# Performance work log

Hardware: AMD Instinct MI355X
Metric: run time of the kernel (lower is better)

## Reference

```python
import jax, jax.numpy as jnp
import numpy as np

N_NODES = 512
IN_FEATURES = 512
N_HEADS = 8
N_HIDDEN = 64  # out_features // n_heads
NEG_SLOPE = 0.2


def setup_inputs() -> dict:
    key = jax.random.key(0)
    k_h, k_ws, k_wt, k_a, k_adj = jax.random.split(key, 5)
    lim_w = 1.0 / np.sqrt(IN_FEATURES)
    lim_a = 1.0 / np.sqrt(N_HIDDEN)
    h = jax.random.normal(k_h, (1, N_NODES, IN_FEATURES), dtype=jnp.float32)
    # nn.Linear weights: [out, in]
    W_source = jax.random.uniform(k_ws, (N_HEADS * N_HIDDEN, IN_FEATURES), jnp.float32, -lim_w, lim_w)
    W_target = jax.random.uniform(k_wt, (N_HEADS * N_HIDDEN, IN_FEATURES), jnp.float32, -lim_w, lim_w)
    attn_w = jax.random.uniform(k_a, (N_HIDDEN,), jnp.float32, -lim_a, lim_a)  # Linear(n_hidden, 1)
    adjacency_matrix = jax.random.randint(k_adj, (N_NODES, N_NODES, 1), 0, 2, dtype=jnp.int32)
    return {"h": h, "W_source": W_source, "W_target": W_target,
            "attn_w": attn_w, "adjacency_matrix": adjacency_matrix}


def reference(h, W_source, W_target, attn_w, adjacency_matrix):
    n_nodes = h.shape[1]
    x = h[0]  # [N, D]; module assumes batch == 1
    g_source = (x @ W_source.T).reshape(n_nodes, N_HEADS, N_HIDDEN)  # [N,H,F]
    g_target = (x @ W_target.T).reshape(n_nodes, N_HEADS, N_HIDDEN)  # [N,H,F]
    # g_sum[i, j] = g_source[j] + g_target[i]  (repeat / repeat_interleave semantics)
    g_sum = g_source[None, :, :, :] + g_target[:, None, :, :]  # [N,N,H,F]
    act = jnp.where(g_sum >= 0, g_sum, NEG_SLOPE * g_sum)       # LeakyReLU
    scores = jnp.einsum('ijhf,f->ijh', act, attn_w)              # [N,N,H]
    scores = jnp.where(adjacency_matrix == 0, -jnp.inf, scores)  # adj broadcasts over heads
    attention = jax.nn.softmax(scores, axis=1)                   # softmax over source nodes j
    # dropout p applied at eval -> identity
    head_output = jnp.einsum('ijh,jhf->ihf', attention, g_target)  # [N,H,F]
    out = head_output.reshape(n_nodes, N_HEADS * N_HIDDEN)         # is_concat=True
    return out, attention
```

## Files before the change

### kernel.cpp

```cpp
#include <hip/hip_runtime.h>

#define NN 512
#define IND 512
#define NH 8
#define NF 64

__global__ __launch_bounds__(256) void transpose512(
    const float* __restrict__ X, float* __restrict__ Xt,
    const float* __restrict__ Wtg, float* __restrict__ Wtg_t)
{
    const float* src = blockIdx.z ? Wtg : X;
    float* dst       = blockIdx.z ? Wtg_t : Xt;
    __shared__ float tile[32][33];
    const int tid = threadIdx.x;
    const int tx = tid & 31, ty4 = (tid >> 5) * 4;
    const int x  = blockIdx.x * 32 + tx;
    const int y0 = blockIdx.y * 32 + ty4;
    #pragma unroll
    for (int r = 0; r < 4; ++r)
        tile[ty4 + r][tx] = src[(size_t)(y0 + r) * NN + x];
    __syncthreads();
    const int xo  = blockIdx.y * 32 + tx;
    const int yo0 = blockIdx.x * 32 + ty4;
    #pragma unroll
    for (int r = 0; r < 4; ++r)
        dst[(size_t)(yo0 + r) * NN + xo] = tile[tx][ty4 + r];
}

__global__ __launch_bounds__(256) void gemm_tn(
    const float* __restrict__ Sa, const float* __restrict__ Va, float* __restrict__ Ca,
    const float* __restrict__ Sb, const float* __restrict__ Vb, float* __restrict__ Cb)
{
    const float* S = blockIdx.z ? Sb : Sa;
    const float* V = blockIdx.z ? Vb : Va;
    float*       C = blockIdx.z ? Cb : Ca;

    __shared__ float2 sp[2][4][64];

    const int tid  = threadIdx.x;
    const int wv   = __builtin_amdgcn_readfirstlane(tid >> 6);
    const int lane = tid & 63;
    const int rg = wv & 1, kh = wv >> 1;
    const int r0 = blockIdx.y * 8 + rg * 4;
    const int c0 = blockIdx.x * 128 + lane * 2;

    const float* Sp = S + (size_t)r0 * IND + kh * 256;
    const float* Vp = V + (size_t)kh * 256 * NN + c0;

    float2 a0 = {0.f, 0.f}, a1 = {0.f, 0.f}, a2 = {0.f, 0.f}, a3 = {0.f, 0.f};
    #pragma unroll 8
    for (int k = 0; k < 256; ++k) {
        float2 v = *reinterpret_cast<const float2*>(Vp + (size_t)k * NN);
        float s0 = Sp[k];
        float s1 = Sp[IND + k];
        float s2 = Sp[2 * IND + k];
        float s3 = Sp[3 * IND + k];
        a0.x = fmaf(s0, v.x, a0.x); a0.y = fmaf(s0, v.y, a0.y);
        a1.x = fmaf(s1, v.x, a1.x); a1.y = fmaf(s1, v.y, a1.y);
        a2.x = fmaf(s2, v.x, a2.x); a2.y = fmaf(s2, v.y, a2.y);
        a3.x = fmaf(s3, v.x, a3.x); a3.y = fmaf(s3, v.y, a3.y);
    }
    if (kh) {
        sp[rg][0][lane] = a0; sp[rg][1][lane] = a1;
        sp[rg][2][lane] = a2; sp[rg][3][lane] = a3;
    }
    __syncthreads();
    if (!kh) {
        float2 p;
        p = sp[rg][0][lane]; a0.x += p.x; a0.y += p.y;
        p = sp[rg][1][lane]; a1.x += p.x; a1.y += p.y;
        p = sp[rg][2][lane]; a2.x += p.x; a2.y += p.y;
        p = sp[rg][3][lane]; a3.x += p.x; a3.y += p.y;
        *reinterpret_cast<float2*>(C + (size_t)(r0 + 0) * NN + c0) = a0;
        *reinterpret_cast<float2*>(C + (size_t)(r0 + 1) * NN + c0) = a1;
        *reinterpret_cast<float2*>(C + (size_t)(r0 + 2) * NN + c0) = a2;
        *reinterpret_cast<float2*>(C + (size_t)(r0 + 3) * NN + c0) = a3;
    }
}

__global__ __launch_bounds__(256) void gat_attn(
    const float* __restrict__ Gs_t,
    const float* __restrict__ Gt,
    const float* __restrict__ attn_w,
    const int*   __restrict__ adj,
    float* __restrict__ out_feat,
    float* __restrict__ out_att)
{
    __shared__ float s_sc[4][512];
    __shared__ float s_red[4][4][64];

    const int tid = threadIdx.x;
    const int i0  = blockIdx.x * 4;
    const int h   = blockIdx.y;

    {
        const int jj = tid * 2;
        float2 acc0 = {0.f,0.f}, acc1 = {0.f,0.f}, acc2 = {0.f,0.f}, acc3 = {0.f,0.f};
        const float* gsp = Gs_t + (size_t)h * NF * NN + jj;
        const float* gtp = Gt + (size_t)i0 * IND + h * NF;
        #pragma unroll 4
        for (int f = 0; f < NF; ++f) {
            float w  = attn_w[f];
            float w6 = 0.6f * w, w4 = 0.4f * w;
            float2 g = *reinterpret_cast<const float2*>(gsp + (size_t)f * NN);
            float gt0 = gtp[f];
            float gt1 = gtp[IND + f];
            float gt2 = gtp[2 * IND + f];
            float gt3 = gtp[3 * IND + f];
            float tx, ty;
            tx = g.x + gt0; ty = g.y + gt0;
            acc0.x = fmaf(w4, fabsf(tx), fmaf(w6, tx, acc0.x));
            acc0.y = fmaf(w4, fabsf(ty), fmaf(w6, ty, acc0.y));
            tx = g.x + gt1; ty = g.y + gt1;
            acc1.x = fmaf(w4, fabsf(tx), fmaf(w6, tx, acc1.x));
            acc1.y = fmaf(w4, fabsf(ty), fmaf(w6, ty, acc1.y));
            tx = g.x + gt2; ty = g.y + gt2;
            acc2.x = fmaf(w4, fabsf(tx), fmaf(w6, tx, acc2.x));
            acc2.y = fmaf(w4, fabsf(ty), fmaf(w6, ty, acc2.y));
            tx = g.x + gt3; ty = g.y + gt3;
            acc3.x = fmaf(w4, fabsf(tx), fmaf(w6, tx, acc3.x));
            acc3.y = fmaf(w4, fabsf(ty), fmaf(w6, ty, acc3.y));
        }
        int2 ad;
        ad = *reinterpret_cast<const int2*>(adj + (size_t)(i0 + 0) * NN + jj);
        s_sc[0][jj]     = ad.x ? acc0.x : -INFINITY;
        s_sc[0][jj + 1] = ad.y ? acc0.y : -INFINITY;
        ad = *reinterpret_cast<const int2*>(adj + (size_t)(i0 + 1) * NN + jj);
        s_sc[1][jj]     = ad.x ? acc1.x : -INFINITY;
        s_sc[1][jj + 1] = ad.y ? acc1.y : -INFINITY;
        ad = *reinterpret_cast<const int2*>(adj + (size_t)(i0 + 2) * NN + jj);
        s_sc[2][jj]     = ad.x ? acc2.x : -INFINITY;
        s_sc[2][jj + 1] = ad.y ? acc2.y : -INFINITY;
        ad = *reinterpret_cast<const int2*>(adj + (size_t)(i0 + 3) * NN + jj);
        s_sc[3][jj]     = ad.x ? acc3.x : -INFINITY;
        s_sc[3][jj + 1] = ad.y ? acc3.y : -INFINITY;
    }
    __syncthreads();

    {
        const int ii = tid >> 6, lane = tid & 63;
        float m = -INFINITY;
        #pragma unroll
        for (int r = 0; r < 8; ++r) m = fmaxf(m, s_sc[ii][lane + r * 64]);
        #pragma unroll
        for (int off = 32; off >= 1; off >>= 1) m = fmaxf(m, __shfl_xor(m, off, 64));
        float e[8];
        float sum = 0.f;
        #pragma unroll
        for (int r = 0; r < 8; ++r) {
            float ev = __expf(s_sc[ii][lane + r * 64] - m);
            e[r] = ev;
            sum += ev;
        }
        #pragma unroll
        for (int off = 32; off >= 1; off >>= 1) sum += __shfl_xor(sum, off, 64);
        float inv = 1.f / sum;
        const int i = i0 + ii;
        #pragma unroll
        for (int r = 0; r < 8; ++r) {
            int j = lane + r * 64;
            float a = e[r] * inv;
            s_sc[ii][j] = a;
            out_att[((size_t)i * NN + j) * NH + h] = a;
        }
    }
    __syncthreads();

    {
        const int w = tid >> 6, lane = tid & 63;
        const int jb = w * 128;
        float o0 = 0.f, o1 = 0.f, o2 = 0.f, o3 = 0.f;
        const float* gtc = Gt + h * NF + lane;
        #pragma unroll 4
        for (int s = 0; s < 32; ++s) {
            const int j = jb + 4 * s;
            float4 b0 = *reinterpret_cast<const float4*>(&s_sc[0][j]);
            float4 b1 = *reinterpret_cast<const float4*>(&s_sc[1][j]);
            float4 b2 = *reinterpret_cast<const float4*>(&s_sc[2][j]);
            float4 b3 = *reinterpret_cast<const float4*>(&s_sc[3][j]);
            float gv;
            gv = gtc[(size_t)(j + 0) * IND];
            o0 = fmaf(b0.x, gv, o0); o1 = fmaf(b1.x, gv, o1);
            o2 = fmaf(b2.x, gv, o2); o3 = fmaf(b3.x, gv, o3);
            gv = gtc[(size_t)(j + 1) * IND];
            o0 = fmaf(b0.y, gv, o0); o1 = fmaf(b1.y, gv, o1);
            o2 = fmaf(b2.y, gv, o2); o3 = fmaf(b3.y, gv, o3);
            gv = gtc[(size_t)(j + 2) * IND];
            o0 = fmaf(b0.z, gv, o0); o1 = fmaf(b1.z, gv, o1);
            o2 = fmaf(b2.z, gv, o2); o3 = fmaf(b3.z, gv, o3);
            gv = gtc[(size_t)(j + 3) * IND];
            o0 = fmaf(b0.w, gv, o0); o1 = fmaf(b1.w, gv, o1);
            o2 = fmaf(b2.w, gv, o2); o3 = fmaf(b3.w, gv, o3);
        }
        s_red[w][0][lane] = o0; s_red[w][1][lane] = o1;
        s_red[w][2][lane] = o2; s_red[w][3][lane] = o3;
    }
    __syncthreads();
    {
        const int ii = tid >> 6, f = tid & 63;
        float s = s_red[0][ii][f] + s_red[1][ii][f] + s_red[2][ii][f] + s_red[3][ii][f];
        out_feat[(size_t)(i0 + ii) * (NH * NF) + h * NF + f] = s;
    }
}

extern "C" void kernel_launch(void* const* d_in, const int* in_sizes, int n_in,
                              void* d_out, int out_size, void* d_ws, size_t ws_size,
                              hipStream_t stream) {
    const float* X   = (const float*)d_in[0];
    const float* Ws  = (const float*)d_in[1];
    const float* Wtg = (const float*)d_in[2];
    const float* aw  = (const float*)d_in[3];
    const int*   adj = (const int*)d_in[4];

    float* Xt    = (float*)d_ws;
    float* Wtg_t = Xt    + (size_t)NN * IND;
    float* Gs_t  = Wtg_t + (size_t)NN * IND;
    float* Gt    = Gs_t  + (size_t)NN * IND;

    float* out_feat = (float*)d_out;
    float* out_att  = out_feat + (size_t)NN * NH * NF;

    hipLaunchKernelGGL(transpose512, dim3(16, 16, 2), dim3(256), 0, stream,
                       X, Xt, Wtg, Wtg_t);
    hipLaunchKernelGGL(gemm_tn, dim3(4, 64, 2), dim3(256), 0, stream,
                       Ws, Xt, Gs_t, X, Wtg_t, Gt);
    hipLaunchKernelGGL(gat_attn, dim3(NN / 4, NH), dim3(256), 0, stream,
                       Gs_t, Gt, aw, adj, out_feat, out_att);
}
```

Before: 108.5 us.

## Fuse transposes into LDS-staged GEMM, simplify LeakyReLU math, pack attention separately

```diff
diff --git a/kernel.cpp b/kernel.cpp
--- a/kernel.cpp
+++ b/kernel.cpp
@@ -5,36 +5,15 @@
 #define NH 8
 #define NF 64
 
-__global__ __launch_bounds__(256) void transpose512(
-    const float* __restrict__ X, float* __restrict__ Xt,
-    const float* __restrict__ Wtg, float* __restrict__ Wtg_t)
+__global__ __launch_bounds__(256) void gemm_nt(
+    const float* __restrict__ Aa, const float* __restrict__ Ba, float* __restrict__ Ca,
+    const float* __restrict__ Ab, const float* __restrict__ Bb, float* __restrict__ Cb)
 {
-    const float* src = blockIdx.z ? Wtg : X;
-    float* dst       = blockIdx.z ? Wtg_t : Xt;
-    __shared__ float tile[32][33];
-    const int tid = threadIdx.x;
-    const int tx = tid & 31, ty4 = (tid >> 5) * 4;
-    const int x  = blockIdx.x * 32 + tx;
-    const int y0 = blockIdx.y * 32 + ty4;
-    #pragma unroll
-    for (int r = 0; r < 4; ++r)
-        tile[ty4 + r][tx] = src[(size_t)(y0 + r) * NN + x];
-    __syncthreads();
-    const int xo  = blockIdx.y * 32 + tx;
-    const int yo0 = blockIdx.x * 32 + ty4;
-    #pragma unroll
-    for (int r = 0; r < 4; ++r)
-        dst[(size_t)(yo0 + r) * NN + xo] = tile[tx][ty4 + r];
-}
-
-__global__ __launch_bounds__(256) void gemm_tn(
-    const float* __restrict__ Sa, const float* __restrict__ Va, float* __restrict__ Ca,
-    const float* __restrict__ Sb, const float* __restrict__ Vb, float* __restrict__ Cb)
-{
-    const float* S = blockIdx.z ? Sb : Sa;
-    const float* V = blockIdx.z ? Vb : Va;
+    const float* A = blockIdx.z ? Ab : Aa;
+    const float* B = blockIdx.z ? Bb : Ba;
     float*       C = blockIdx.z ? Cb : Ca;
 
+    __shared__ __align__(16) float Vs[2][32][132];
     __shared__ float2 sp[2][4][64];
 
     const int tid  = threadIdx.x;
@@ -42,24 +21,43 @@
     const int lane = tid & 63;
     const int rg = wv & 1, kh = wv >> 1;
     const int r0 = blockIdx.y * 8 + rg * 4;
-    const int c0 = blockIdx.x * 128 + lane * 2;
-
-    const float* Sp = S + (size_t)r0 * IND + kh * 256;
-    const float* Vp = V + (size_t)kh * 256 * NN + c0;
-
-    float2 a0 = {0.f, 0.f}, a1 = {0.f, 0.f}, a2 = {0.f, 0.f}, a3 = {0.f, 0.f};
-    #pragma unroll 8
-    for (int k = 0; k < 256; ++k) {
-        float2 v = *reinterpret_cast<const float2*>(Vp + (size_t)k * NN);
-        float s0 = Sp[k];
-        float s1 = Sp[IND + k];
-        float s2 = Sp[2 * IND + k];
-        float s3 = Sp[3 * IND + k];
-        a0.x = fmaf(s0, v.x, a0.x); a0.y = fmaf(s0, v.y, a0.y);
-        a1.x = fmaf(s1, v.x, a1.x); a1.y = fmaf(s1, v.y, a1.y);
-        a2.x = fmaf(s2, v.x, a2.x); a2.y = fmaf(s2, v.y, a2.y);
-        a3.x = fmaf(s3, v.x, a3.x); a3.y = fmaf(s3, v.y, a3.y);
-    }
+    const int c0 = blockIdx.x * 128;
+
+    const float* Sp = A + (size_t)r0 * IND + kh * 256;
+    const int ts = tid & 127;
+    const float* Brow = B + (size_t)(c0 + ts) * IND + kh * 256;
+
+    float2 a0 = {0.f,0.f}, a1 = {0.f,0.f}, a2 = {0.f,0.f}, a3 = {0.f,0.f};
+
+    for (int ch = 0; ch < 8; ++ch) {
+        float4 f[8];
+        const float4* bp = reinterpret_cast<const float4*>(Brow + ch * 32);
+        #pragma unroll
+        for (int i = 0; i < 8; ++i) f[i] = bp[i];
+        __syncthreads();
+        #pragma unroll
+        for (int i = 0; i < 8; ++i) {
+            Vs[kh][i * 4 + 0][ts] = f[i].x;
+            Vs[kh][i * 4 + 1][ts] = f[i].y;
+            Vs[kh][i * 4 + 2][ts] = f[i].z;
+            Vs[kh][i * 4 + 3][ts] = f[i].w;
+        }
+        __syncthreads();
+        const float* Spc = Sp + ch * 32;
+        #pragma unroll 8
+        for (int kk = 0; kk < 32; ++kk) {
+            float2 v = *reinterpret_cast<const float2*>(&Vs[kh][kk][lane * 2]);
+            float s0 = Spc[kk];
+            float s1 = Spc[IND + kk];
+            float s2 = Spc[2 * IND + kk];
+            float s3 = Spc[3 * IND + kk];
+            a0.x = fmaf(s0, v.x, a0.x); a0.y = fmaf(s0, v.y, a0.y);
+            a1.x = fmaf(s1, v.x, a1.x); a1.y = fmaf(s1, v.y, a1.y);
+            a2.x = fmaf(s2, v.x, a2.x); a2.y = fmaf(s2, v.y, a2.y);
+            a3.x = fmaf(s3, v.x, a3.x); a3.y = fmaf(s3, v.y, a3.y);
+        }
+    }
+
     if (kh) {
         sp[rg][0][lane] = a0; sp[rg][1][lane] = a1;
         sp[rg][2][lane] = a2; sp[rg][3][lane] = a3;
@@ -67,14 +65,15 @@
     __syncthreads();
     if (!kh) {
         float2 p;
+        const int cc = c0 + lane * 2;
         p = sp[rg][0][lane]; a0.x += p.x; a0.y += p.y;
         p = sp[rg][1][lane]; a1.x += p.x; a1.y += p.y;
         p = sp[rg][2][lane]; a2.x += p.x; a2.y += p.y;
         p = sp[rg][3][lane]; a3.x += p.x; a3.y += p.y;
-        *reinterpret_cast<float2*>(C + (size_t)(r0 + 0) * NN + c0) = a0;
-        *reinterpret_cast<float2*>(C + (size_t)(r0 + 1) * NN + c0) = a1;
-        *reinterpret_cast<float2*>(C + (size_t)(r0 + 2) * NN + c0) = a2;
-        *reinterpret_cast<float2*>(C + (size_t)(r0 + 3) * NN + c0) = a3;
+        *reinterpret_cast<float2*>(C + (size_t)(r0 + 0) * NN + cc) = a0;
+        *reinterpret_cast<float2*>(C + (size_t)(r0 + 1) * NN + cc) = a1;
+        *reinterpret_cast<float2*>(C + (size_t)(r0 + 2) * NN + cc) = a2;
+        *reinterpret_cast<float2*>(C + (size_t)(r0 + 3) * NN + cc) = a3;
     }
 }
 
@@ -84,7 +83,7 @@
     const float* __restrict__ attn_w,
     const int*   __restrict__ adj,
     float* __restrict__ out_feat,
-    float* __restrict__ out_att)
+    float* __restrict__ att_ws)
 {
     __shared__ float s_sc[4][512];
     __shared__ float s_red[4][4][64];
@@ -96,44 +95,43 @@
     {
         const int jj = tid * 2;
         float2 acc0 = {0.f,0.f}, acc1 = {0.f,0.f}, acc2 = {0.f,0.f}, acc3 = {0.f,0.f};
+        float2 p = {0.f,0.f};
         const float* gsp = Gs_t + (size_t)h * NF * NN + jj;
         const float* gtp = Gt + (size_t)i0 * IND + h * NF;
         #pragma unroll 4
         for (int f = 0; f < NF; ++f) {
             float w  = attn_w[f];
-            float w6 = 0.6f * w, w4 = 0.4f * w;
             float2 g = *reinterpret_cast<const float2*>(gsp + (size_t)f * NN);
             float gt0 = gtp[f];
             float gt1 = gtp[IND + f];
             float gt2 = gtp[2 * IND + f];
             float gt3 = gtp[3 * IND + f];
+            p.x = fmaf(w, g.x, p.x);
+            p.y = fmaf(w, g.y, p.y);
             float tx, ty;
             tx = g.x + gt0; ty = g.y + gt0;
-            acc0.x = fmaf(w4, fabsf(tx), fmaf(w6, tx, acc0.x));
-            acc0.y = fmaf(w4, fabsf(ty), fmaf(w6, ty, acc0.y));
+            acc0.x = fmaf(w, fabsf(tx), acc0.x); acc0.y = fmaf(w, fabsf(ty), acc0.y);
             tx = g.x + gt1; ty = g.y + gt1;
-            acc1.x = fmaf(w4, fabsf(tx), fmaf(w6, tx, acc1.x));
-            acc1.y = fmaf(w4, fabsf(ty), fmaf(w6, ty, acc1.y));
+            acc1.x = fmaf(w, fabsf(tx), acc1.x); acc1.y = fmaf(w, fabsf(ty), acc1.y);
             tx = g.x + gt2; ty = g.y + gt2;
-            acc2.x = fmaf(w4, fabsf(tx), fmaf(w6, tx, acc2.x));
-            acc2.y = fmaf(w4, fabsf(ty), fmaf(w6, ty, acc2.y));
+            acc2.x = fmaf(w, fabsf(tx), acc2.x); acc2.y = fmaf(w, fabsf(ty), acc2.y);
             tx = g.x + gt3; ty = g.y + gt3;
-            acc3.x = fmaf(w4, fabsf(tx), fmaf(w6, tx, acc3.x));
-            acc3.y = fmaf(w4, fabsf(ty), fmaf(w6, ty, acc3.y));
-        }
+            acc3.x = fmaf(w, fabsf(tx), acc3.x); acc3.y = fmaf(w, fabsf(ty), acc3.y);
+        }
+        const float px = 0.6f * p.x, py = 0.6f * p.y;
         int2 ad;
         ad = *reinterpret_cast<const int2*>(adj + (size_t)(i0 + 0) * NN + jj);
-        s_sc[0][jj]     = ad.x ? acc0.x : -INFINITY;
-        s_sc[0][jj + 1] = ad.y ? acc0.y : -INFINITY;
+        s_sc[0][jj]     = ad.x ? fmaf(0.4f, acc0.x, px) : -INFINITY;
+        s_sc[0][jj + 1] = ad.y ? fmaf(0.4f, acc0.y, py) : -INFINITY;
         ad = *reinterpret_cast<const int2*>(adj + (size_t)(i0 + 1) * NN + jj);
-        s_sc[1][jj]     = ad.x ? acc1.x : -INFINITY;
-        s_sc[1][jj + 1] = ad.y ? acc1.y : -INFINITY;
+        s_sc[1][jj]     = ad.x ? fmaf(0.4f, acc1.x, px) : -INFINITY;
+        s_sc[1][jj + 1] = ad.y ? fmaf(0.4f, acc1.y, py) : -INFINITY;
         ad = *reinterpret_cast<const int2*>(adj + (size_t)(i0 + 2) * NN + jj);
-        s_sc[2][jj]     = ad.x ? acc2.x : -INFINITY;
-        s_sc[2][jj + 1] = ad.y ? acc2.y : -INFINITY;
+        s_sc[2][jj]     = ad.x ? fmaf(0.4f, acc2.x, px) : -INFINITY;
+        s_sc[2][jj + 1] = ad.y ? fmaf(0.4f, acc2.y, py) : -INFINITY;
         ad = *reinterpret_cast<const int2*>(adj + (size_t)(i0 + 3) * NN + jj);
-        s_sc[3][jj]     = ad.x ? acc3.x : -INFINITY;
-        s_sc[3][jj + 1] = ad.y ? acc3.y : -INFINITY;
+        s_sc[3][jj]     = ad.x ? fmaf(0.4f, acc3.x, px) : -INFINITY;
+        s_sc[3][jj + 1] = ad.y ? fmaf(0.4f, acc3.y, py) : -INFINITY;
     }
     __syncthreads();
 
@@ -156,12 +154,13 @@
         for (int off = 32; off >= 1; off >>= 1) sum += __shfl_xor(sum, off, 64);
         float inv = 1.f / sum;
         const int i = i0 + ii;
+        float* awp = att_ws + ((size_t)h * NN + i) * NN;
         #pragma unroll
         for (int r = 0; r < 8; ++r) {
             int j = lane + r * 64;
             float a = e[r] * inv;
             s_sc[ii][j] = a;
-            out_att[((size_t)i * NN + j) * NH + h] = a;
+            awp[j] = a;
         }
     }
     __syncthreads();
@@ -203,6 +202,28 @@
     }
 }
 
+__global__ __launch_bounds__(256) void att_pack(
+    const float* __restrict__ att_ws, float* __restrict__ out_att)
+{
+    const int tid = threadIdx.x;
+    const int i0  = blockIdx.x * 2;
+    const int jj  = tid * 2;
+    #pragma unroll
+    for (int ii = 0; ii < 2; ++ii) {
+        const int i = i0 + ii;
+        float2 v[8];
+        #pragma unroll
+        for (int h = 0; h < 8; ++h)
+            v[h] = *reinterpret_cast<const float2*>(att_ws + ((size_t)h * NN + i) * NN + jj);
+        float4* dst = reinterpret_cast<float4*>(out_att + ((size_t)i * NN + jj) * NH);
+        float4 o;
+        o.x = v[0].x; o.y = v[1].x; o.z = v[2].x; o.w = v[3].x; dst[0] = o;
+        o.x = v[4].x; o.y = v[5].x; o.z = v[6].x; o.w = v[7].x; dst[1] = o;
+        o.x = v[0].y; o.y = v[1].y; o.z = v[2].y; o.w = v[3].y; dst[2] = o;
+        o.x = v[4].y; o.y = v[5].y; o.z = v[6].y; o.w = v[7].y; dst[3] = o;
+    }
+}
+
 extern "C" void kernel_launch(void* const* d_in, const int* in_sizes, int n_in,
                               void* d_out, int out_size, void* d_ws, size_t ws_size,
                               hipStream_t stream) {
@@ -212,18 +233,17 @@
     const float* aw  = (const float*)d_in[3];
     const int*   adj = (const int*)d_in[4];
 
-    float* Xt    = (float*)d_ws;
-    float* Wtg_t = Xt    + (size_t)NN * IND;
-    float* Gs_t  = Wtg_t + (size_t)NN * IND;
-    float* Gt    = Gs_t  + (size_t)NN * IND;
+    float* Gs_t   = (float*)d_ws;
+    float* Gt     = Gs_t   + (size_t)NN * IND;
+    float* att_ws = Gt     + (size_t)NN * IND;
 
     float* out_feat = (float*)d_out;
     float* out_att  = out_feat + (size_t)NN * NH * NF;
 
-    hipLaunchKernelGGL(transpose512, dim3(16, 16, 2), dim3(256), 0, stream,
-                       X, Xt, Wtg, Wtg_t);
-    hipLaunchKernelGGL(gemm_tn, dim3(4, 64, 2), dim3(256), 0, stream,
-                       Ws, Xt, Gs_t, X, Wtg_t, Gt);
+    hipLaunchKernelGGL(gemm_nt, dim3(4, 64, 2), dim3(256), 0, stream,
+                       Ws, X, Gs_t, X, Wtg, Gt);
     hipLaunchKernelGGL(gat_attn, dim3(NN / 4, NH), dim3(256), 0, stream,
-                       Gs_t, Gt, aw, adj, out_feat, out_att);
-}
+                       Gs_t, Gt, aw, adj, out_feat, att_ws);
+    hipLaunchKernelGGL(att_pack, dim3(NN / 2), dim3(256), 0, stream,
+                       att_ws, out_att);
+}
```

Measured after the change: 110.1 us. Within noise of the previous version (+1.5%).
